# Kernel optimization log

Hardware: AMD Instinct MI355X
Metric: run time of the kernel (lower is better)

Reference implementation:

```python
import jax, jax.numpy as jnp
import numpy as np
from jax import lax

FS = 250
FREQS = np.arange(1.0, 41.0)  # 40 frequencies, 1..40 Hz
NCH = 32
NCYC = 6.0

def _kernel_size():
    f_min = float(FREQS.min())
    cyc = max(2.0, NCYC * (f_min / 4.0)) if f_min < 4.0 else NCYC
    sigma_max = cyc / (2.0 * np.pi * f_min)
    K = int(8 * sigma_max * FS)
    if K % 2 == 0:
        K += 1
    return K

def _morlet_weights():
    K = _kernel_size()
    t = np.linspace(-K / 2 / FS, K / 2 / FS, K)
    w = np.zeros((len(FREQS), 2, K), dtype=np.float32)
    for i, f in enumerate(FREQS):
        if f < 1.0:
            cycles = 3.0 + f * (4.0 - 3.0)
        elif f < 4.0:
            cycles = 4.0 + (f - 1.0) / 3.0 * (6.0 - 4.0)
        else:
            cycles = NCYC
        sigma = cycles / (2.0 * np.pi * f)
        wav = np.exp(2j * np.pi * f * t) * np.exp(-t ** 2 / (2 * sigma ** 2))
        wav = wav / np.linalg.norm(wav)
        w[i, 0] = np.real(wav)
        w[i, 1] = np.imag(wav)
    # per-channel layout: [f0_real, f0_imag, f1_real, ...] repeated for each of NCH groups
    W = np.tile(w[None], (NCH, 1, 1, 1)).reshape(NCH * len(FREQS) * 2, 1, K)
    return jnp.asarray(W)

# fixed 7x5 electrode grid mapping (channels 0..31)
_MAP = np.array([[-1, 0, -1, 1, -1], [2, 3, 4, 5, 6], [7, 8, 13, 9, 10],
                 [11, 12, 18, 14, 15], [16, 17, 19, 20, 21],
                 [22, 23, 24, 25, 26], [27, 28, 29, 30, 31]])
ROWS = np.array([np.where(_MAP == c)[0][0] for c in range(32)])
COLS = np.array([np.where(_MAP == c)[1][0] for c in range(32)])


def setup_inputs() -> dict:
    key = jax.random.key(0)
    x = jax.random.normal(key, (8, 32, 2000), dtype=jnp.float32)
    return {"x": x, "W": _morlet_weights()}


def reference(x, W):
    B, C, T = x.shape
    F = W.shape[0] // (C * 2)
    pad = W.shape[-1] // 2
    # reflect padding (padding_mode='reflect') then VALID grouped conv (groups=C)
    xp = jnp.pad(x, ((0, 0), (0, 0), (pad, pad)), mode='reflect')
    y = lax.conv_general_dilated(
        xp, W, window_strides=(1,), padding='VALID',
        dimension_numbers=('NCH', 'OIH', 'NCH'), feature_group_count=C)
    y = y.reshape(B, C, F, 2, T)
    real = y[:, :, :, 0, :]
    imag = y[:, :, :, 1, :]
    mag = jnp.sqrt(real * real + imag * imag)
    phase = jnp.arctan2(imag, real)
    features = jnp.stack([mag, phase], axis=-1)          # [B, C, F, T, 2]
    features = jnp.transpose(features, (0, 4, 2, 1, 3))  # [B, 2, F, C, T]
    canvas = jnp.zeros((B, 2, F, 7, 5, T), dtype=x.dtype)
    canvas = canvas.at[:, :, :, ROWS, COLS, :].set(features)  # [B, 2, F, 7, 5, T]
    return canvas
```

## Files before the change

kernel.cpp:

```cpp
#include <hip/hip_runtime.h>
#include <math.h>

#define NB 8
#define NC 32
#define NF 40
#define NT 2000
#define KW 637
#define PADW 318
#define TPB 256
#define HALFT 1000
#define XLN  (NT + 2 * PADW)
#define XLNP 2656
#define WMAX 2720
#define FG 8
#define NFG (NF / FG)

#define XSIZE (NB * NC * NT)
#define KC 320

#define DET  3e-4f
#define DET2 1e-7f

__device__ __constant__ int POS[32] = {
  1,3,5,6,7,8,9,10,11,13,14,15,16,12,18,19,20,21,17,22,23,24,25,26,
  27,28,29,30,31,32,33,34
};

__global__ __launch_bounds__(TPB)
void cwt_zero_holes(float* __restrict__ out) {
  int row = blockIdx.x;
  int p = (row % 3) * 2;
  int rest = row / 3;
  size_t base = ((size_t)rest * 35 + p) * NT;
  float4 z = make_float4(0.f, 0.f, 0.f, 0.f);
  for (int t = threadIdx.x * 4; t < NT; t += TPB * 4)
    *(float4*)&out[base + t] = z;
}

__device__ __noinline__ float2 fixup_point(const float* __restrict__ xv,
                                           const float* __restrict__ wr,
                                           const float* __restrict__ wi) {
  float b0r = 0.f, b0i = 0.f;
  #pragma unroll 4
  for (int k = 0; k < KC; ++k) {
    const float v = xv[k];
    b0r = __fadd_rn(b0r, __fmul_rn(wr[k], v));
    b0i = __fadd_rn(b0i, __fmul_rn(wi[k], v));
  }
  float b1r = 0.f, b1i = 0.f;
  #pragma unroll 4
  for (int k = KC; k < KW; ++k) {
    const float v = xv[k];
    b1r = __fadd_rn(b1r, __fmul_rn(wr[k], v));
    b1i = __fadd_rn(b1i, __fmul_rn(wi[k], v));
  }
  const float re = __fadd_rn(b0r, b1r);
  const float im = __fadd_rn(b0i, b1i);
  return make_float2(sqrtf(__fadd_rn(__fmul_rn(re, re), __fmul_rn(im, im))),
                     atan2f(im, re));
}

__device__ __forceinline__ void support_window(int fi, int& klo, int& kend,
                                               int& Lp) {
  const float cyc = (fi == 0) ? 4.0f
                  : (fi == 1) ? (4.0f + 2.0f / 3.0f)
                  : (fi == 2) ? (4.0f + 4.0f / 3.0f) : 6.0f;
  const float sigma = cyc / (6.283185307179586f * (float)(fi + 1));
  int h = (int)ceilf(6.0f * sigma * 250.0f);
  if (h > PADW) h = PADW;
  klo  = (PADW - h) & ~3;
  kend = PADW + h + 1;
  Lp   = (kend - klo + 3) & ~3;
}

__global__ __launch_bounds__(TPB)
void cwt_fast(const float* __restrict__ x,
              const float* __restrict__ W,
              float* __restrict__ out) {
  __shared__ __align__(16) float xp[XLNP];
  __shared__ __align__(16) float wlds[WMAX];

  const int bid = blockIdx.x;
  const int r   = bid & (FG - 1);
  const int q   = bid >> 3;
  const int g   = (q + r) & (FG - 1);
  const int b   = q >> 5;
  const int c   = q & 31;
  const int tid = threadIdx.x;

  const float* __restrict__ xrow = x + (size_t)(b * NC + c) * NT;

  for (int i = tid; i < XLNP; i += TPB) {
    float v = 0.f;
    if (i < XLN) {
      int s = i - PADW;
      int m = (s < 0) ? -s : ((s >= NT) ? (2 * NT - 2 - s) : s);
      v = xrow[m];
    }
    xp[i] = v;
  }

  {
    int woff = 0;
    for (int j = 0; j < NFG; ++j) {
      const int fi = g + FG * j;
      int klo, kend, Lp;
      support_window(fi, klo, kend, Lp);
      const float* __restrict__ wr_g = W + (size_t)(2 * fi) * KW;
      const float* __restrict__ wi_g = wr_g + KW;
      for (int i = tid; i < Lp; i += TPB) {
        const int k = klo + i;
        const bool in = k < kend;
        wlds[woff + i]      = in ? wr_g[k] : 0.f;
        wlds[woff + Lp + i] = in ? wi_g[k] : 0.f;
      }
      woff += 2 * Lp;
    }
  }
  __syncthreads();

  const bool active = (tid < HALFT / 4);
  const int ta = tid * 4;
  const int tb = tid * 4 + HALFT;
  const int pos = POS[c];
  const float4* __restrict__ xp4 = (const float4*)xp;

  int woff = 0;
  for (int j = 0; j < NFG; ++j) {
    const int fi = g + FG * j;
    int klo, kend, Lp;
    support_window(fi, klo, kend, Lp);
    const float* __restrict__ wr = wlds + woff;
    const float* __restrict__ wi = wr + Lp;
    woff += 2 * Lp;
    if (!active) continue;

    const int nst = Lp >> 2;
    const int ia0 = (ta + klo) >> 2;
    const int ib0 = (tb + klo) >> 2;
    float4 a0 = xp4[ia0], a1 = xp4[ia0 + 1];
    float4 b0 = xp4[ib0], b1 = xp4[ib0 + 1];

    float rea[4] = {0.f,0.f,0.f,0.f}, ima[4] = {0.f,0.f,0.f,0.f};
    float reb[4] = {0.f,0.f,0.f,0.f}, imb[4] = {0.f,0.f,0.f,0.f};

    #pragma unroll 2
    for (int s = 0; s < nst; ++s) {
      const float4 wr4 = ((const float4*)wr)[s];
      const float4 wi4 = ((const float4*)wi)[s];
      const float4 a2 = xp4[ia0 + s + 2];
      const float4 b2 = xp4[ib0 + s + 2];
      const float va[8] = {a0.x,a0.y,a0.z,a0.w, a1.x,a1.y,a1.z,a1.w};
      const float vb[8] = {b0.x,b0.y,b0.z,b0.w, b1.x,b1.y,b1.z,b1.w};
      const float wrA[4] = {wr4.x, wr4.y, wr4.z, wr4.w};
      const float wiA[4] = {wi4.x, wi4.y, wi4.z, wi4.w};
      #pragma unroll
      for (int u = 0; u < 4; ++u) {
        #pragma unroll
        for (int qq = 0; qq < 4; ++qq) {
          rea[qq] = __fmaf_rn(va[u + qq], wrA[u], rea[qq]);
          ima[qq] = __fmaf_rn(va[u + qq], wiA[u], ima[qq]);
          reb[qq] = __fmaf_rn(vb[u + qq], wrA[u], reb[qq]);
          imb[qq] = __fmaf_rn(vb[u + qq], wiA[u], imb[qq]);
        }
      }
      a0 = a1; a1 = a2; b0 = b1; b1 = b2;
    }

    const size_t magbase = ((size_t)((2*b + 0) * NF + fi) * 35 + pos) * NT;
    const size_t phbase  = ((size_t)((2*b + 1) * NF + fi) * 35 + pos) * NT;
    const float* __restrict__ wr_gf = W + (size_t)(2 * fi) * KW;
    const float* __restrict__ wi_gf = wr_gf + KW;

    {
      float4 mag, ph;
      float* mp = &mag.x; float* pp = &ph.x;
      mag.x = sqrtf(rea[0]*rea[0] + ima[0]*ima[0]);
      mag.y = sqrtf(rea[1]*rea[1] + ima[1]*ima[1]);
      mag.z = sqrtf(rea[2]*rea[2] + ima[2]*ima[2]);
      mag.w = sqrtf(rea[3]*rea[3] + ima[3]*ima[3]);
      ph.x = atan2f(ima[0], rea[0]);
      ph.y = atan2f(ima[1], rea[1]);
      ph.z = atan2f(ima[2], rea[2]);
      ph.w = atan2f(ima[3], rea[3]);
      #pragma unroll
      for (int qq = 0; qq < 4; ++qq) {
        const float a = rea[qq], bb = ima[qq];
        if ((fabsf(bb) < DET && a < 0.f) || (a * a + bb * bb < DET2)) {
          float2 rr = fixup_point(xp + ta + qq, wr_gf, wi_gf);
          mp[qq] = rr.x; pp[qq] = rr.y;
        }
      }
      *(float4*)&out[magbase + ta] = mag;
      *(float4*)&out[phbase  + ta] = ph;
    }
    {
      float4 mag, ph;
      float* mp = &mag.x; float* pp = &ph.x;
      mag.x = sqrtf(reb[0]*reb[0] + imb[0]*imb[0]);
      mag.y = sqrtf(reb[1]*reb[1] + imb[1]*imb[1]);
      mag.z = sqrtf(reb[2]*reb[2] + imb[2]*imb[2]);
      mag.w = sqrtf(reb[3]*reb[3] + imb[3]*imb[3]);
      ph.x = atan2f(imb[0], reb[0]);
      ph.y = atan2f(imb[1], reb[1]);
      ph.z = atan2f(imb[2], reb[2]);
      ph.w = atan2f(imb[3], reb[3]);
      #pragma unroll
      for (int qq = 0; qq < 4; ++qq) {
        const float a = reb[qq], bb = imb[qq];
        if ((fabsf(bb) < DET && a < 0.f) || (a * a + bb * bb < DET2)) {
          float2 rr = fixup_point(xp + tb + qq, wr_gf, wi_gf);
          mp[qq] = rr.x; pp[qq] = rr.y;
        }
      }
      *(float4*)&out[magbase + tb] = mag;
      *(float4*)&out[phbase  + tb] = ph;
    }
  }
}

extern "C" void kernel_launch(void* const* d_in, const int* in_sizes, int n_in,
                              void* d_out, int out_size, void* d_ws, size_t ws_size,
                              hipStream_t stream) {
  const void* xin = d_in[0];
  const void* win = (n_in > 1) ? d_in[1] : d_in[0];
  if (n_in >= 2) {
    if (in_sizes[0] == XSIZE)      { xin = d_in[0]; win = d_in[1]; }
    else if (in_sizes[1] == XSIZE) { xin = d_in[1]; win = d_in[0]; }
  }
  const float* x = (const float*)xin;
  const float* W = (const float*)win;
  float* out = (float*)d_out;

  cwt_zero_holes<<<dim3(NB * 2 * NF * 3), dim3(TPB), 0, stream>>>(out);
  cwt_fast<<<dim3(NB * NC * FG), dim3(TPB), 0, stream>>>(x, W, out);
}
```

Measured before the change: 499.3 us.

## Use packed FP32 FMA with interleaved real/imag weights and 8 outputs per thread

Stores the wavelet weights in LDS as interleaved (real, imag) pairs so one v_pk_fma_f32 updates both the real and imaginary accumulators of an output point, with the input sample broadcast through op_sel. Each thread now computes 8 contiguous outputs instead of two groups of 4, which changes the register blocking and the sliding window of LDS loads. The intent is to halve the VALU FMA instruction count and reduce LDS reads per FMA. The trade-offs are inline asm, higher register pressure, and a zero-padded weight buffer that the lookahead loads read past the window end.

```diff
diff --git a/kernel.cpp b/kernel.cpp
--- a/kernel.cpp
+++ b/kernel.cpp
@@ -8,10 +8,9 @@
 #define KW 637
 #define PADW 318
 #define TPB 256
-#define HALFT 1000
 #define XLN  (NT + 2 * PADW)
 #define XLNP 2656
-#define WMAX 2720
+#define WPMAX 1364
 #define FG 8
 #define NFG (NF / FG)
 
@@ -20,11 +19,22 @@
 
 #define DET  3e-4f
 #define DET2 1e-7f
+
+typedef float f32x2 __attribute__((ext_vector_type(2)));
 
 __device__ __constant__ int POS[32] = {
   1,3,5,6,7,8,9,10,11,13,14,15,16,12,18,19,20,21,17,22,23,24,25,26,
   27,28,29,30,31,32,33,34
 };
+
+__device__ __forceinline__ void pk_fma_b0(f32x2& acc, f32x2 va, f32x2 w) {
+  asm("v_pk_fma_f32 %0, %1, %2, %0 op_sel_hi:[0,1,1]"
+      : "+v"(acc) : "v"(va), "v"(w));
+}
+__device__ __forceinline__ void pk_fma_b1(f32x2& acc, f32x2 va, f32x2 w) {
+  asm("v_pk_fma_f32 %0, %1, %2, %0 op_sel:[1,0,0] op_sel_hi:[1,1,1]"
+      : "+v"(acc) : "v"(va), "v"(w));
+}
 
 __global__ __launch_bounds__(TPB)
 void cwt_zero_holes(float* __restrict__ out) {
@@ -78,7 +88,7 @@
               const float* __restrict__ W,
               float* __restrict__ out) {
   __shared__ __align__(16) float xp[XLNP];
-  __shared__ __align__(16) float wlds[WMAX];
+  __shared__ __align__(16) f32x2 wl2[WPMAX];
 
   const int bid = blockIdx.x;
   const int r   = bid & (FG - 1);
@@ -101,7 +111,7 @@
   }
 
   {
-    int woff = 0;
+    int woffp = 0;
     for (int j = 0; j < NFG; ++j) {
       const int fi = g + FG * j;
       int klo, kend, Lp;
@@ -111,60 +121,68 @@
       for (int i = tid; i < Lp; i += TPB) {
         const int k = klo + i;
         const bool in = k < kend;
-        wlds[woff + i]      = in ? wr_g[k] : 0.f;
-        wlds[woff + Lp + i] = in ? wi_g[k] : 0.f;
+        f32x2 p;
+        p.x = in ? wr_g[k] : 0.f;
+        p.y = in ? wi_g[k] : 0.f;
+        wl2[woffp + i] = p;
       }
-      woff += 2 * Lp;
+      woffp += Lp;
+    }
+    for (int i = woffp + tid; i < WPMAX; i += TPB) {
+      f32x2 z; z.x = 0.f; z.y = 0.f;
+      wl2[i] = z;
     }
   }
   __syncthreads();
 
-  const bool active = (tid < HALFT / 4);
-  const int ta = tid * 4;
-  const int tb = tid * 4 + HALFT;
+  const bool active = (tid < NT / 8);
+  const int ta = tid * 8;
   const int pos = POS[c];
   const float4* __restrict__ xp4 = (const float4*)xp;
 
-  int woff = 0;
+  int woffp = 0;
   for (int j = 0; j < NFG; ++j) {
     const int fi = g + FG * j;
     int klo, kend, Lp;
     support_window(fi, klo, kend, Lp);
-    const float* __restrict__ wr = wlds + woff;
-    const float* __restrict__ wi = wr + Lp;
-    woff += 2 * Lp;
+    const float4* __restrict__ wq4 = (const float4*)(wl2 + woffp);
+    woffp += Lp;
     if (!active) continue;
 
     const int nst = Lp >> 2;
-    const int ia0 = (ta + klo) >> 2;
-    const int ib0 = (tb + klo) >> 2;
-    float4 a0 = xp4[ia0], a1 = xp4[ia0 + 1];
-    float4 b0 = xp4[ib0], b1 = xp4[ib0 + 1];
-
-    float rea[4] = {0.f,0.f,0.f,0.f}, ima[4] = {0.f,0.f,0.f,0.f};
-    float reb[4] = {0.f,0.f,0.f,0.f}, imb[4] = {0.f,0.f,0.f,0.f};
-
-    #pragma unroll 2
+    const float4* __restrict__ xq = xp4 + ((ta + klo) >> 2);
+
+    float4 r0 = xq[0], r1 = xq[1], r2 = xq[2], r3 = xq[3];
+    float4 w0 = wq4[0], w1 = wq4[1], w2 = wq4[2], w3 = wq4[3];
+
+    f32x2 acc[8];
+    #pragma unroll
+    for (int qq = 0; qq < 8; ++qq) { acc[qq].x = 0.f; acc[qq].y = 0.f; }
+
+    #pragma unroll 4
     for (int s = 0; s < nst; ++s) {
-      const float4 wr4 = ((const float4*)wr)[s];
-      const float4 wi4 = ((const float4*)wi)[s];
-      const float4 a2 = xp4[ia0 + s + 2];
-      const float4 b2 = xp4[ib0 + s + 2];
-      const float va[8] = {a0.x,a0.y,a0.z,a0.w, a1.x,a1.y,a1.z,a1.w};
-      const float vb[8] = {b0.x,b0.y,b0.z,b0.w, b1.x,b1.y,b1.z,b1.w};
-      const float wrA[4] = {wr4.x, wr4.y, wr4.z, wr4.w};
-      const float wiA[4] = {wi4.x, wi4.y, wi4.z, wi4.w};
+      const float4 rn  = xq[s + 4];
+      const float4 wn0 = wq4[2 * s + 4];
+      const float4 wn1 = wq4[2 * s + 5];
+
+      f32x2 P[6], WT[4];
+      P[0].x = r0.x; P[0].y = r0.y;  P[1].x = r0.z; P[1].y = r0.w;
+      P[2].x = r1.x; P[2].y = r1.y;  P[3].x = r1.z; P[3].y = r1.w;
+      P[4].x = r2.x; P[4].y = r2.y;  P[5].x = r2.z; P[5].y = r2.w;
+      WT[0].x = w0.x; WT[0].y = w0.y;  WT[1].x = w0.z; WT[1].y = w0.w;
+      WT[2].x = w1.x; WT[2].y = w1.y;  WT[3].x = w1.z; WT[3].y = w1.w;
+
       #pragma unroll
       for (int u = 0; u < 4; ++u) {
         #pragma unroll
-        for (int qq = 0; qq < 4; ++qq) {
-          rea[qq] = __fmaf_rn(va[u + qq], wrA[u], rea[qq]);
-          ima[qq] = __fmaf_rn(va[u + qq], wiA[u], ima[qq]);
-          reb[qq] = __fmaf_rn(vb[u + qq], wrA[u], reb[qq]);
-          imb[qq] = __fmaf_rn(vb[u + qq], wiA[u], imb[qq]);
+        for (int qq = 0; qq < 8; ++qq) {
+          const int jj = u + qq;
+          if (jj & 1) pk_fma_b1(acc[qq], P[jj >> 1], WT[u]);
+          else        pk_fma_b0(acc[qq], P[jj >> 1], WT[u]);
         }
       }
-      a0 = a1; a1 = a2; b0 = b1; b1 = b2;
+      r0 = r1; r1 = r2; r2 = r3; r3 = rn;
+      w0 = w2; w1 = w3; w2 = wn0; w3 = wn1;
     }
 
     const size_t magbase = ((size_t)((2*b + 0) * NF + fi) * 35 + pos) * NT;
@@ -172,50 +190,21 @@
     const float* __restrict__ wr_gf = W + (size_t)(2 * fi) * KW;
     const float* __restrict__ wi_gf = wr_gf + KW;
 
-    {
-      float4 mag, ph;
-      float* mp = &mag.x; float* pp = &ph.x;
-      mag.x = sqrtf(rea[0]*rea[0] + ima[0]*ima[0]);
-      mag.y = sqrtf(rea[1]*rea[1] + ima[1]*ima[1]);
-      mag.z = sqrtf(rea[2]*rea[2] + ima[2]*ima[2]);
-      mag.w = sqrtf(rea[3]*rea[3] + ima[3]*ima[3]);
-      ph.x = atan2f(ima[0], rea[0]);
-      ph.y = atan2f(ima[1], rea[1]);
-      ph.z = atan2f(ima[2], rea[2]);
-      ph.w = atan2f(ima[3], rea[3]);
-      #pragma unroll
-      for (int qq = 0; qq < 4; ++qq) {
-        const float a = rea[qq], bb = ima[qq];
-        if ((fabsf(bb) < DET && a < 0.f) || (a * a + bb * bb < DET2)) {
-          float2 rr = fixup_point(xp + ta + qq, wr_gf, wi_gf);
-          mp[qq] = rr.x; pp[qq] = rr.y;
-        }
+    float mg[8], ph[8];
+    #pragma unroll
+    for (int qq = 0; qq < 8; ++qq) {
+      const float a = acc[qq].x, bb = acc[qq].y;
+      mg[qq] = sqrtf(a * a + bb * bb);
+      ph[qq] = atan2f(bb, a);
+      if ((fabsf(bb) < DET && a < 0.f) || (a * a + bb * bb < DET2)) {
+        float2 rr = fixup_point(xp + ta + qq, wr_gf, wi_gf);
+        mg[qq] = rr.x; ph[qq] = rr.y;
       }
-      *(float4*)&out[magbase + ta] = mag;
-      *(float4*)&out[phbase  + ta] = ph;
-    }
-    {
-      float4 mag, ph;
-      float* mp = &mag.x; float* pp = &ph.x;
-      mag.x = sqrtf(reb[0]*reb[0] + imb[0]*imb[0]);
-      mag.y = sqrtf(reb[1]*reb[1] + imb[1]*imb[1]);
-      mag.z = sqrtf(reb[2]*reb[2] + imb[2]*imb[2]);
-      mag.w = sqrtf(reb[3]*reb[3] + imb[3]*imb[3]);
-      ph.x = atan2f(imb[0], reb[0]);
-      ph.y = atan2f(imb[1], reb[1]);
-      ph.z = atan2f(imb[2], reb[2]);
-      ph.w = atan2f(imb[3], reb[3]);
-      #pragma unroll
-      for (int qq = 0; qq < 4; ++qq) {
-        const float a = reb[qq], bb = imb[qq];
-        if ((fabsf(bb) < DET && a < 0.f) || (a * a + bb * bb < DET2)) {
-          float2 rr = fixup_point(xp + tb + qq, wr_gf, wi_gf);
-          mp[qq] = rr.x; pp[qq] = rr.y;
-        }
-      }
-      *(float4*)&out[magbase + tb] = mag;
-      *(float4*)&out[phbase  + tb] = ph;
-    }
+    }
+    *(float4*)&out[magbase + ta]     = make_float4(mg[0], mg[1], mg[2], mg[3]);
+    *(float4*)&out[magbase + ta + 4] = make_float4(mg[4], mg[5], mg[6], mg[7]);
+    *(float4*)&out[phbase  + ta]     = make_float4(ph[0], ph[1], ph[2], ph[3]);
+    *(float4*)&out[phbase  + ta + 4] = make_float4(ph[4], ph[5], ph[6], ph[7]);
   }
 }
 
```

Measured after the change: 478.4 us. 4.2% less time.
